# Performance work log

Hardware: AMD Instinct MI355X
Metric: run time of the kernel (lower is better)

The kernel has to match this reference:

```python
import jax, jax.numpy as jnp
import numpy as np

D_MODEL = 1024
NUM_HEADS = 16
HEAD_DIM = D_MODEL // NUM_HEADS  # 64
N = 1024
B = 8


def setup_inputs() -> dict:
    key = jax.random.key(0)
    ks = jax.random.split(key, 11)
    s = 0.02
    inp = {
        'query': jax.random.normal(ks[0], (B, D_MODEL, N), jnp.float32),
        'key':   jax.random.normal(ks[1], (B, D_MODEL, N), jnp.float32),
        'value': jax.random.normal(ks[2], (B, D_MODEL, N), jnp.float32),
        # 1x1 conv1d == linear over channel dim: weight [out, in], bias [out]
        'Wq': jax.random.normal(ks[3], (D_MODEL, D_MODEL), jnp.float32) * s,
        'bq': jax.random.normal(ks[4], (D_MODEL,), jnp.float32) * s,
        'Wk': jax.random.normal(ks[5], (D_MODEL, D_MODEL), jnp.float32) * s,
        'bk': jax.random.normal(ks[6], (D_MODEL,), jnp.float32) * s,
        'Wv': jax.random.normal(ks[7], (D_MODEL, D_MODEL), jnp.float32) * s,
        'bv': jax.random.normal(ks[8], (D_MODEL,), jnp.float32) * s,
        'Wm': jax.random.normal(ks[9], (D_MODEL, D_MODEL), jnp.float32) * s,
        'bm': jax.random.normal(ks[10], (D_MODEL,), jnp.float32) * s,
    }
    return inp


def _proj(W, b, x):
    # nn.Conv1d(kernel_size=1): out[b,o,n] = sum_i W[o,i] x[b,i,n] + b[o]
    return jnp.einsum('oi,bin->bon', W, x) + b[None, :, None]


def reference(query, key, value, Wq, bq, Wk, bk, Wv, bv, Wm, bm):
    Bd = query.shape[0]
    # view(B, dim, heads, N): channel axis split as (head_dim, num_heads)
    q = _proj(Wq, bq, query).reshape(Bd, HEAD_DIM, NUM_HEADS, -1)
    k = _proj(Wk, bk, key).reshape(Bd, HEAD_DIM, NUM_HEADS, -1)
    v = _proj(Wv, bv, value).reshape(Bd, HEAD_DIM, NUM_HEADS, -1)
    scale = 1.0 / (HEAD_DIM ** 0.5)
    scores = jnp.einsum('bdhn,bdhm->bhnm', q, k) * scale  # [B,H,N,N]
    prob = jax.nn.softmax(scores, axis=-1)
    x = jnp.einsum('bhnm,bdhm->bdhn', prob, v)  # [B,D,H,N]
    out = _proj(Wm, bm, x.reshape(Bd, HEAD_DIM * NUM_HEADS, -1))
    return out
```

## Files before the change

kernel.cpp:

```cpp
#include <hip/hip_runtime.h>

typedef __bf16 bf16x8 __attribute__((ext_vector_type(8)));
typedef __bf16 bf16x4 __attribute__((ext_vector_type(4)));
typedef float f32x4 __attribute__((ext_vector_type(4)));
typedef unsigned short u16;
typedef unsigned int u32;

typedef union { bf16x8 v8; bf16x4 v4[2]; } bfu;

__device__ __forceinline__ u16 f2bf(float f) {
  u32 u = __builtin_bit_cast(u32, f);
  u = (u + 0x7FFFu + ((u >> 16) & 1u)) >> 16;
  return (u16)u;
}

__device__ __forceinline__ void gload_lds16(const void* g, void* l) {
  __builtin_amdgcn_global_load_lds((const __attribute__((address_space(1))) void*)g,
                                   (__attribute__((address_space(3))) void*)l, 16, 0, 0);
}

__global__ __launch_bounds__(256) void transpose_cast3(const float* __restrict__ q,
                                                       const float* __restrict__ k,
                                                       const float* __restrict__ v,
                                                       u16* __restrict__ X3) {
  __shared__ float T[64][68];
  int tid = threadIdx.x;
  int n0 = blockIdx.x * 64, i0 = blockIdx.y * 64;
  int z = blockIdx.z;
  int which = z >> 3, b = z & 7;
  const float* src = (which == 0) ? q : (which == 1) ? k : v;
  size_t boff = (size_t)b << 20;
  const float* s = src + boff;
  u16* d = X3 + ((size_t)which << 23) + boff;
  int ir = tid >> 4, n4 = (tid & 15) * 4;
#pragma unroll
  for (int r = 0; r < 4; ++r) {
    int i_loc = ir + r * 16;
    float4 vv = *(const float4*)(s + (size_t)(i0 + i_loc) * 1024 + n0 + n4);
    *(float4*)&T[i_loc][n4] = vv;
  }
  __syncthreads();
  int nr = tid >> 3, i8 = (tid & 7) * 8;
#pragma unroll
  for (int r = 0; r < 2; ++r) {
    int n_loc = nr + r * 32;
    u32 pk[4];
#pragma unroll
    for (int j = 0; j < 4; ++j) {
      float f0 = T[i8 + 2 * j][n_loc];
      float f1 = T[i8 + 2 * j + 1][n_loc];
      pk[j] = (u32)f2bf(f0) | ((u32)f2bf(f1) << 16);
    }
    *(uint4*)(d + (size_t)(n0 + n_loc) * 1024 + i0 + i8) = make_uint4(pk[0], pk[1], pk[2], pk[3]);
  }
}

__global__ __launch_bounds__(256) void transpose_cast(const float* __restrict__ src,
                                                      u16* __restrict__ dst) {
  __shared__ float T[64][68];
  int tid = threadIdx.x;
  int n0 = blockIdx.x * 64, i0 = blockIdx.y * 64;
  size_t boff = (size_t)blockIdx.z << 20;
  const float* s = src + boff;
  u16* d = dst + boff;
  int ir = tid >> 4, n4 = (tid & 15) * 4;
#pragma unroll
  for (int r = 0; r < 4; ++r) {
    int i_loc = ir + r * 16;
    float4 v = *(const float4*)(s + (size_t)(i0 + i_loc) * 1024 + n0 + n4);
    *(float4*)&T[i_loc][n4] = v;
  }
  __syncthreads();
  int nr = tid >> 3, i8 = (tid & 7) * 8;
#pragma unroll
  for (int r = 0; r < 2; ++r) {
    int n_loc = nr + r * 32;
    u32 pk[4];
#pragma unroll
    for (int j = 0; j < 4; ++j) {
      float f0 = T[i8 + 2 * j][n_loc];
      float f1 = T[i8 + 2 * j + 1][n_loc];
      pk[j] = (u32)f2bf(f0) | ((u32)f2bf(f1) << 16);
    }
    *(uint4*)(d + (size_t)(n0 + n_loc) * 1024 + i0 + i8) = make_uint4(pk[0], pk[1], pk[2], pk[3]);
  }
}

__global__ __launch_bounds__(256) void cast_weights(const float* __restrict__ Wq,
                                                    const float* __restrict__ Wk,
                                                    const float* __restrict__ Wv,
                                                    const float* __restrict__ Wm,
                                                    u16* __restrict__ out) {
  int w = blockIdx.y;
  const float* src = (w == 0) ? Wq : (w == 1) ? Wk : (w == 2) ? Wv : Wm;
  u16* dst = out + ((size_t)w << 20);
  int o = blockIdx.x;
  int c4 = threadIdx.x * 4;
  float f[4];
  if (w < 3) {
    float4 v = *(const float4*)(src + (size_t)o * 1024 + c4);
    f[0] = v.x; f[1] = v.y; f[2] = v.z; f[3] = v.w;
  } else {
#pragma unroll
    for (int j = 0; j < 4; ++j) {
      int cp = c4 + j;
      f[j] = src[(size_t)o * 1024 + (cp & 63) * 16 + (cp >> 6)];
    }
  }
  u32 p0 = (u32)f2bf(f[0]) | ((u32)f2bf(f[1]) << 16);
  u32 p1 = (u32)f2bf(f[2]) | ((u32)f2bf(f[3]) << 16);
  *(uint2*)(dst + (size_t)o * 1024 + c4) = make_uint2(p0, p1);
}

__device__ __forceinline__ void gemm_body(const u16* __restrict__ A,
                                          const u16* __restrict__ B,
                                          const float* __restrict__ bias,
                                          void* __restrict__ Out, float escale,
                                          int epi, u16* LD) {
  int tid = threadIdx.x;
  int wave = tid >> 6, l = tid & 63, ln = l & 15, g = l >> 4;
  int wm = wave >> 2, wn = wave & 3;
  int bid = blockIdx.x;
  int mt = (bid >> 3) & 7;
  int nt = ((bid & 7) << 2) | (bid >> 6);
  int c0 = mt * 128, n0 = nt * 256;

  int R = tid >> 3, sl = tid & 7;
  int v = sl ^ (R & 7);
  int sa = v >> 2, sg = v & 3;
  const u16* aSrc = A + (size_t)(c0 + 2 * R + sa) * 1024 + sg * 8;
  const u16* bSrc0 = B + (size_t)(n0 + 2 * R + sa) * 1024 + sg * 8;
  const u16* bSrc1 = B + (size_t)(n0 + 128 + 2 * R + sa) * 1024 + sg * 8;

  int slr = ((((ln & 1) << 2) | g) ^ ((ln >> 1) & 7)) * 8;
  int laneA = (wm * 32 + (ln >> 1)) * 64 + slr;
  int laneB = (wn * 32 + (ln >> 1)) * 64 + slr;

  f32x4 acc[4][4] = {};

#define STAGE(buf, kt)                                                   \
  do {                                                                   \
    gload_lds16(aSrc + (kt) * 32, &LD[(buf) * 4096 + tid * 8]);          \
    gload_lds16(bSrc0 + (kt) * 32, &LD[16384 + (buf) * 8192 + tid * 8]); \
    gload_lds16(bSrc1 + (kt) * 32,                                       \
                &LD[16384 + (buf) * 8192 + 4096 + tid * 8]);             \
  } while (0)

  STAGE(0, 0);
  STAGE(1, 1);
  STAGE(2, 2);

#pragma unroll
  for (int t = 0; t < 32; ++t) {
    if (t < 30)
      asm volatile("s_waitcnt vmcnt(6)" ::: "memory");
    else if (t == 30)
      asm volatile("s_waitcnt vmcnt(3)" ::: "memory");
    else
      asm volatile("s_waitcnt vmcnt(0)" ::: "memory");
    asm volatile("s_barrier" ::: "memory");
    if (t <= 28) STAGE((t + 3) & 3, t + 3);
    const int ab = (t & 3) * 4096;
    const int bb = 16384 + (t & 3) * 8192;
    bf16x8 af[4], bfr[4];
#pragma unroll
    for (int mm = 0; mm < 4; ++mm) af[mm] = *(const bf16x8*)&LD[ab + laneA + mm * 512];
#pragma unroll
    for (int nn = 0; nn < 4; ++nn) bfr[nn] = *(const bf16x8*)&LD[bb + laneB + nn * 512];
    __builtin_amdgcn_s_setprio(1);
#pragma unroll
    for (int mm = 0; mm < 4; ++mm)
#pragma unroll
      for (int nn = 0; nn < 4; ++nn)
        acc[mm][nn] = __builtin_amdgcn_mfma_f32_16x16x32_bf16(af[mm], bfr[nn], acc[mm][nn], 0, 0, 0);
    __builtin_amdgcn_s_setprio(0);
  }
#undef STAGE

  int D0 = (c0 >> 4) + wm * 4;
#pragma unroll
  for (int nn = 0; nn < 4; ++nn) {
    size_t ng = (size_t)n0 + wn * 64 + nn * 16 + ln;
#pragma unroll
    for (int r = 0; r < 4; ++r) {
      int h = g * 4 + r;
      if (epi == 0) {
        bf16x4 pk;
#pragma unroll
        for (int mm = 0; mm < 4; ++mm) {
          int c = c0 + wm * 64 + mm * 16 + h;
          pk[mm] = (__bf16)((acc[mm][nn][r] + bias[c]) * escale);
        }
        *(bf16x4*)((u16*)Out + ng * 1024 + (size_t)h * 64 + D0) = pk;
      } else {
        size_t b = ng >> 10, n = ng & 1023;
#pragma unroll
        for (int mm = 0; mm < 4; ++mm) {
          int c = c0 + wm * 64 + mm * 16 + h;
          float val = (acc[mm][nn][r] + bias[c]) * escale;
          if (epi == 1) {
            int d = D0 + mm;
            ((u16*)Out)[((b * 16 + h) * 64 + d) * 1024 + n] = f2bf(val);
          } else {
            ((float*)Out)[(b << 20) + (size_t)c * 1024 + n] = val;
          }
        }
      }
    }
  }
}

template <int EPI>
__global__ __launch_bounds__(512, 2) void gemm4b(const u16* __restrict__ A,
                                                 const u16* __restrict__ B,
                                                 const float* __restrict__ bias,
                                                 void* __restrict__ Out, float escale) {
  __shared__ u16 LD[49152];
  gemm_body(A, B, bias, Out, escale, EPI, LD);
}

__global__ __launch_bounds__(512, 2) void gemm_qkv(const u16* __restrict__ Wbf,
                                                   const u16* __restrict__ X3,
                                                   const float* __restrict__ bq,
                                                   const float* __restrict__ bk,
                                                   const float* __restrict__ bv,
                                                   u16* __restrict__ Qh,
                                                   u16* __restrict__ Kh,
                                                   u16* __restrict__ Vt, float qscale) {
  __shared__ u16 LD[49152];
  int z = blockIdx.y;
  const u16* A = Wbf + ((size_t)z << 20);
  const u16* B = X3 + ((size_t)z << 23);
  const float* bias = (z == 0) ? bq : (z == 1) ? bk : bv;
  void* Out = (z == 0) ? (void*)Qh : (z == 1) ? (void*)Kh : (void*)Vt;
  float escale = (z == 0) ? qscale : 1.0f;
  int epi = (z == 2) ? 1 : 0;
  gemm_body(A, B, bias, Out, escale, epi, LD);
}

__global__ __launch_bounds__(256, 4) void attn_kernel(const u16* __restrict__ Qh,
                                                      const u16* __restrict__ Kh,
                                                      const u16* __restrict__ Vt,
                                                      u16* __restrict__ Xh) {
  __shared__ u16 Ks[2][4096];
  __shared__ u16 Vs[2][4096];
  int tid = threadIdx.x;
  int w = tid >> 6, l = tid & 63, ln = l & 15, g = l >> 4;
  int id = blockIdx.x;
  int qp = (id & 63) >> 3;
  int bh = ((id >> 6) << 3) | (id & 7);
  size_t b = bh >> 4;
  int h = bh & 15;
  const u16* Qg = Qh + (b << 20) + (h << 6);
  const u16* Kg = Kh + (b << 20) + (h << 6);
  const u16* Vg = Vt + ((size_t)bh << 16);
  u16* Og = Xh + (b << 20) + (h << 6);

  bf16x8 qf[2][2];
#pragma unroll
  for (int t = 0; t < 2; ++t)
#pragma unroll
    for (int kk = 0; kk < 2; ++kk)
      qf[t][kk] = *(const bf16x8*)(Qg + (size_t)(qp * 128 + t * 64 + w * 16 + ln) * 1024 + kk * 32 + g * 8);

  int lr = l >> 3;
  int sw8 = ((l & 7) ^ lr) << 3;
  int r0 = w * 16 + lr, r1 = r0 + 8;
  const u16* kS0 = Kg + (size_t)r0 * 1024 + sw8;
  const u16* kS1 = Kg + (size_t)r1 * 1024 + sw8;
  const u16* vS0 = Vg + (size_t)r0 * 1024 + sw8;
  const u16* vS1 = Vg + (size_t)r1 * 1024 + sw8;

  f32x4 xacc[2][4] = {};
  float lacc[2] = {0.f, 0.f};

  gload_lds16(kS0, &Ks[0][(w * 2) * 512]);
  gload_lds16(kS1, &Ks[0][(w * 2 + 1) * 512]);
  gload_lds16(vS0, &Vs[0][(w * 2) * 512]);
  gload_lds16(vS1, &Vs[0][(w * 2 + 1) * 512]);
  __syncthreads();

  int sx = ln & 7;
  int cur = 0;
  for (int kt = 0; kt < 16; ++kt) {
    if (kt < 15) {
      int nxt = cur ^ 1;
      gload_lds16(kS0 + (size_t)(kt + 1) * 65536, &Ks[nxt][(w * 2) * 512]);
      gload_lds16(kS1 + (size_t)(kt + 1) * 65536, &Ks[nxt][(w * 2 + 1) * 512]);
      gload_lds16(vS0 + (kt + 1) * 64, &Vs[nxt][(w * 2) * 512]);
      gload_lds16(vS1 + (kt + 1) * 64, &Vs[nxt][(w * 2 + 1) * 512]);
    }
    bf16x8 kf[2][4];
#pragma unroll
    for (int kk = 0; kk < 2; ++kk)
#pragma unroll
      for (int f = 0; f < 4; ++f) {
        int slot = (((kk << 2) + g) ^ sx) << 3;
        kf[kk][f] = *(const bf16x8*)&Ks[cur][(f * 16 + ln) * 64 + slot];
      }
    bf16x8 vf[2][4];
#pragma unroll
    for (int kk = 0; kk < 2; ++kk) {
      int s0 = (kk << 2) + (g >> 1);
      int off = (g & 1) << 2;
#pragma unroll
      for (int fd = 0; fd < 4; ++fd) {
        int rowb = (fd * 16 + ln) * 64;
        bfu uv;
        uv.v4[0] = *(const bf16x4*)&Vs[cur][rowb + ((s0 ^ sx) << 3) + off];
        uv.v4[1] = *(const bf16x4*)&Vs[cur][rowb + (((s0 + 2) ^ sx) << 3) + off];
        vf[kk][fd] = uv.v8;
      }
    }
    f32x4 sacc[2][4] = {};
#pragma unroll
    for (int t = 0; t < 2; ++t)
#pragma unroll
      for (int kk = 0; kk < 2; ++kk)
#pragma unroll
        for (int f = 0; f < 4; ++f)
          sacc[t][f] = __builtin_amdgcn_mfma_f32_16x16x32_bf16(kf[kk][f], qf[t][kk], sacc[t][f], 0, 0, 0);
#pragma unroll
    for (int t = 0; t < 2; ++t) {
      bf16x8 pf[2];
#pragma unroll
      for (int kk = 0; kk < 2; ++kk) {
        bfu up;
#pragma unroll
        for (int e2 = 0; e2 < 2; ++e2) {
          int f = 2 * kk + e2;
          float p0 = __builtin_amdgcn_exp2f(sacc[t][f][0]);
          float p1 = __builtin_amdgcn_exp2f(sacc[t][f][1]);
          float p2 = __builtin_amdgcn_exp2f(sacc[t][f][2]);
          float p3 = __builtin_amdgcn_exp2f(sacc[t][f][3]);
          lacc[t] += (p0 + p1) + (p2 + p3);
          bf16x4 pb;
          pb[0] = (__bf16)p0; pb[1] = (__bf16)p1; pb[2] = (__bf16)p2; pb[3] = (__bf16)p3;
          up.v4[e2] = pb;
        }
        pf[kk] = up.v8;
      }
#pragma unroll
      for (int kk = 0; kk < 2; ++kk)
#pragma unroll
        for (int fd = 0; fd < 4; ++fd)
          xacc[t][fd] = __builtin_amdgcn_mfma_f32_16x16x32_bf16(pf[kk], vf[kk][fd], xacc[t][fd], 0, 0, 0);
    }
    __syncthreads();
    cur ^= 1;
  }

#pragma unroll
  for (int t = 0; t < 2; ++t) {
    float lt = lacc[t];
    lt += __shfl_xor(lt, 16);
    lt += __shfl_xor(lt, 32);
    float il[4];
#pragma unroll
    for (int r = 0; r < 4; ++r) il[r] = 1.0f / __shfl(lt, g * 4 + r);
#pragma unroll
    for (int fd = 0; fd < 4; ++fd)
#pragma unroll
      for (int r = 0; r < 4; ++r) {
        int nq = qp * 128 + t * 64 + w * 16 + g * 4 + r;
        Og[(size_t)nq * 1024 + fd * 16 + ln] = f2bf(xacc[t][fd][r] * il[r]);
      }
  }
}

extern "C" void kernel_launch(void* const* d_in, const int* in_sizes, int n_in,
                              void* d_out, int out_size, void* d_ws, size_t ws_size,
                              hipStream_t stream) {
  const float* q  = (const float*)d_in[0];
  const float* k  = (const float*)d_in[1];
  const float* v  = (const float*)d_in[2];
  const float* Wq = (const float*)d_in[3];
  const float* bq = (const float*)d_in[4];
  const float* Wk = (const float*)d_in[5];
  const float* bk = (const float*)d_in[6];
  const float* Wv = (const float*)d_in[7];
  const float* bv = (const float*)d_in[8];
  const float* Wm = (const float*)d_in[9];
  const float* bm = (const float*)d_in[10];

  char* ws = (char*)d_ws;
  u16* Wbf = (u16*)ws;
  u16* Qh  = (u16*)(ws + (8ull << 20));
  u16* Kh  = (u16*)(ws + (24ull << 20));
  u16* Vt  = (u16*)(ws + (40ull << 20));
  u16* X3  = (u16*)(ws + (56ull << 20));

  cast_weights<<<dim3(1024, 4, 1), 256, 0, stream>>>(Wq, Wk, Wv, Wm, Wbf);

  const float qscale = 0.125f * 1.44269504088896340736f;

  if (ws_size >= (104ull << 20)) {
    transpose_cast3<<<dim3(16, 16, 24), 256, 0, stream>>>(q, k, v, X3);
    gemm_qkv<<<dim3(256, 3), 512, 0, stream>>>(Wbf, X3, bq, bk, bv, Qh, Kh, Vt, qscale);
  } else {
    dim3 tg(16, 16, 8);
    transpose_cast<<<tg, 256, 0, stream>>>(q, X3);
    gemm4b<0><<<256, 512, 0, stream>>>(Wbf, X3, bq, Qh, qscale);
    transpose_cast<<<tg, 256, 0, stream>>>(k, X3);
    gemm4b<0><<<256, 512, 0, stream>>>(Wbf + (1u << 20), X3, bk, Kh, 1.0f);
    transpose_cast<<<tg, 256, 0, stream>>>(v, X3);
    gemm4b<1><<<256, 512, 0, stream>>>(Wbf + (2u << 20), X3, bv, Vt, 1.0f);
  }

  attn_kernel<<<1024, 256, 0, stream>>>(Qh, Kh, Vt, X3);

  gemm4b<2><<<256, 512, 0, stream>>>(Wbf + (3u << 20), X3, bm, d_out, 1.0f);
}
```

Baseline: 180.8 us.

## Enlarge GEMM tiles to 256x256 with new LDS swizzle and halved grid

Switches the projection GEMMs from 128x256 to 256x256 output tiles per block, doubling A-side staging and accumulators per wave (8x4 MFMA tiles) and reworking the LDS swizzle and tile-to-block mapping. The aim is more operand reuse per LDS load and fewer global loads per FLOP. In exchange it halves the number of blocks to 128 per GEMM, raises LDS use to 128KB per block, and increases register pressure. Together these can reduce occupancy and leave many CUs idle.

```diff
diff --git a/kernel.cpp b/kernel.cpp
--- a/kernel.cpp
+++ b/kernel.cpp
@@ -112,72 +112,73 @@
   *(uint2*)(dst + (size_t)o * 1024 + c4) = make_uint2(p0, p1);
 }
 
-__device__ __forceinline__ void gemm_body(const u16* __restrict__ A,
-                                          const u16* __restrict__ B,
-                                          const float* __restrict__ bias,
-                                          void* __restrict__ Out, float escale,
-                                          int epi, u16* LD) {
+__device__ __forceinline__ void gemm256_body(const u16* __restrict__ A,
+                                             const u16* __restrict__ B,
+                                             const float* __restrict__ bias,
+                                             void* __restrict__ Out, float escale,
+                                             int epi, u16* LD) {
   int tid = threadIdx.x;
   int wave = tid >> 6, l = tid & 63, ln = l & 15, g = l >> 4;
   int wm = wave >> 2, wn = wave & 3;
   int bid = blockIdx.x;
-  int mt = (bid >> 3) & 7;
-  int nt = ((bid & 7) << 2) | (bid >> 6);
-  int c0 = mt * 128, n0 = nt * 256;
-
-  int R = tid >> 3, sl = tid & 7;
-  int v = sl ^ (R & 7);
-  int sa = v >> 2, sg = v & 3;
-  const u16* aSrc = A + (size_t)(c0 + 2 * R + sa) * 1024 + sg * 8;
-  const u16* bSrc0 = B + (size_t)(n0 + 2 * R + sa) * 1024 + sg * 8;
-  const u16* bSrc1 = B + (size_t)(n0 + 128 + 2 * R + sa) * 1024 + sg * 8;
-
-  int slr = ((((ln & 1) << 2) | g) ^ ((ln >> 1) & 7)) * 8;
-  int laneA = (wm * 32 + (ln >> 1)) * 64 + slr;
-  int laneB = (wn * 32 + (ln >> 1)) * 64 + slr;
-
-  f32x4 acc[4][4] = {};
-
-#define STAGE(buf, kt)                                                   \
+  int work = (bid & 7) * 16 + (bid >> 3);
+  int mt = work >> 5, nt = work & 31;
+  int c0 = mt * 256, n0 = nt * 256;
+
+  int r0 = tid >> 2, cs = tid & 3;
+  int col0 = (cs ^ ((r0 & 3) ^ ((r0 >> 2) & 3))) * 8;
+  const u16* aS0 = A + (size_t)(c0 + r0) * 1024 + col0;
+  const u16* aS1 = A + (size_t)(c0 + 128 + r0) * 1024 + col0;
+  const u16* bS0 = B + (size_t)(n0 + r0) * 1024 + col0;
+  const u16* bS1 = B + (size_t)(n0 + 128 + r0) * 1024 + col0;
+
+  int sl = (g ^ (ln & 3) ^ ((ln >> 2) & 3)) * 8;
+  int laneA = (wm * 128 + ln) * 32 + sl;
+  int laneB = (wn * 64 + ln) * 32 + sl;
+
+  f32x4 acc[8][4] = {};
+
+#define STG(buf, kt)                                                     \
   do {                                                                   \
-    gload_lds16(aSrc + (kt) * 32, &LD[(buf) * 4096 + tid * 8]);          \
-    gload_lds16(bSrc0 + (kt) * 32, &LD[16384 + (buf) * 8192 + tid * 8]); \
-    gload_lds16(bSrc1 + (kt) * 32,                                       \
-                &LD[16384 + (buf) * 8192 + 4096 + tid * 8]);             \
+    gload_lds16(aS0 + (kt) * 32, &LD[(buf) * 8192 + tid * 8]);           \
+    gload_lds16(aS1 + (kt) * 32, &LD[(buf) * 8192 + 4096 + tid * 8]);    \
+    gload_lds16(bS0 + (kt) * 32, &LD[32768 + (buf) * 8192 + tid * 8]);   \
+    gload_lds16(bS1 + (kt) * 32,                                         \
+                &LD[32768 + (buf) * 8192 + 4096 + tid * 8]);             \
   } while (0)
 
-  STAGE(0, 0);
-  STAGE(1, 1);
-  STAGE(2, 2);
+  STG(0, 0);
+  STG(1, 1);
+  STG(2, 2);
 
 #pragma unroll
   for (int t = 0; t < 32; ++t) {
     if (t < 30)
-      asm volatile("s_waitcnt vmcnt(6)" ::: "memory");
+      asm volatile("s_waitcnt vmcnt(8)" ::: "memory");
     else if (t == 30)
-      asm volatile("s_waitcnt vmcnt(3)" ::: "memory");
+      asm volatile("s_waitcnt vmcnt(4)" ::: "memory");
     else
       asm volatile("s_waitcnt vmcnt(0)" ::: "memory");
     asm volatile("s_barrier" ::: "memory");
-    if (t <= 28) STAGE((t + 3) & 3, t + 3);
-    const int ab = (t & 3) * 4096;
-    const int bb = 16384 + (t & 3) * 8192;
-    bf16x8 af[4], bfr[4];
-#pragma unroll
-    for (int mm = 0; mm < 4; ++mm) af[mm] = *(const bf16x8*)&LD[ab + laneA + mm * 512];
+    if (t <= 28) STG((t + 3) & 3, t + 3);
+    const int ab = (t & 3) * 8192;
+    const int bb = 32768 + (t & 3) * 8192;
+    bf16x8 bfr[4];
 #pragma unroll
     for (int nn = 0; nn < 4; ++nn) bfr[nn] = *(const bf16x8*)&LD[bb + laneB + nn * 512];
     __builtin_amdgcn_s_setprio(1);
 #pragma unroll
-    for (int mm = 0; mm < 4; ++mm)
+    for (int mm = 0; mm < 8; ++mm) {
+      bf16x8 af = *(const bf16x8*)&LD[ab + laneA + mm * 512];
 #pragma unroll
       for (int nn = 0; nn < 4; ++nn)
-        acc[mm][nn] = __builtin_amdgcn_mfma_f32_16x16x32_bf16(af[mm], bfr[nn], acc[mm][nn], 0, 0, 0);
+        acc[mm][nn] = __builtin_amdgcn_mfma_f32_16x16x32_bf16(af, bfr[nn], acc[mm][nn], 0, 0, 0);
+    }
     __builtin_amdgcn_s_setprio(0);
   }
-#undef STAGE
-
-  int D0 = (c0 >> 4) + wm * 4;
+#undef STG
+
+  int D0 = (c0 >> 4) + wm * 8;
 #pragma unroll
   for (int nn = 0; nn < 4; ++nn) {
     size_t ng = (size_t)n0 + wn * 64 + nn * 16 + ln;
@@ -185,18 +186,18 @@
     for (int r = 0; r < 4; ++r) {
       int h = g * 4 + r;
       if (epi == 0) {
-        bf16x4 pk;
-#pragma unroll
-        for (int mm = 0; mm < 4; ++mm) {
-          int c = c0 + wm * 64 + mm * 16 + h;
+        bf16x8 pk;
+#pragma unroll
+        for (int mm = 0; mm < 8; ++mm) {
+          int c = c0 + wm * 128 + mm * 16 + h;
           pk[mm] = (__bf16)((acc[mm][nn][r] + bias[c]) * escale);
         }
-        *(bf16x4*)((u16*)Out + ng * 1024 + (size_t)h * 64 + D0) = pk;
+        *(bf16x8*)((u16*)Out + ng * 1024 + (size_t)h * 64 + D0) = pk;
       } else {
         size_t b = ng >> 10, n = ng & 1023;
 #pragma unroll
-        for (int mm = 0; mm < 4; ++mm) {
-          int c = c0 + wm * 64 + mm * 16 + h;
+        for (int mm = 0; mm < 8; ++mm) {
+          int c = c0 + wm * 128 + mm * 16 + h;
           float val = (acc[mm][nn][r] + bias[c]) * escale;
           if (epi == 1) {
             int d = D0 + mm;
@@ -211,12 +212,12 @@
 }
 
 template <int EPI>
-__global__ __launch_bounds__(512, 2) void gemm4b(const u16* __restrict__ A,
-                                                 const u16* __restrict__ B,
-                                                 const float* __restrict__ bias,
-                                                 void* __restrict__ Out, float escale) {
-  __shared__ u16 LD[49152];
-  gemm_body(A, B, bias, Out, escale, EPI, LD);
+__global__ __launch_bounds__(512, 2) void gemm256(const u16* __restrict__ A,
+                                                  const u16* __restrict__ B,
+                                                  const float* __restrict__ bias,
+                                                  void* __restrict__ Out, float escale) {
+  __shared__ u16 LD[65536];
+  gemm256_body(A, B, bias, Out, escale, EPI, LD);
 }
 
 __global__ __launch_bounds__(512, 2) void gemm_qkv(const u16* __restrict__ Wbf,
@@ -227,7 +228,7 @@
                                                    u16* __restrict__ Qh,
                                                    u16* __restrict__ Kh,
                                                    u16* __restrict__ Vt, float qscale) {
-  __shared__ u16 LD[49152];
+  __shared__ u16 LD[65536];
   int z = blockIdx.y;
   const u16* A = Wbf + ((size_t)z << 20);
   const u16* B = X3 + ((size_t)z << 23);
@@ -235,7 +236,7 @@
   void* Out = (z == 0) ? (void*)Qh : (z == 1) ? (void*)Kh : (void*)Vt;
   float escale = (z == 0) ? qscale : 1.0f;
   int epi = (z == 2) ? 1 : 0;
-  gemm_body(A, B, bias, Out, escale, epi, LD);
+  gemm256_body(A, B, bias, Out, escale, epi, LD);
 }
 
 __global__ __launch_bounds__(256, 4) void attn_kernel(const u16* __restrict__ Qh,
@@ -396,18 +397,18 @@
 
   if (ws_size >= (104ull << 20)) {
     transpose_cast3<<<dim3(16, 16, 24), 256, 0, stream>>>(q, k, v, X3);
-    gemm_qkv<<<dim3(256, 3), 512, 0, stream>>>(Wbf, X3, bq, bk, bv, Qh, Kh, Vt, qscale);
+    gemm_qkv<<<dim3(128, 3), 512, 0, stream>>>(Wbf, X3, bq, bk, bv, Qh, Kh, Vt, qscale);
   } else {
     dim3 tg(16, 16, 8);
     transpose_cast<<<tg, 256, 0, stream>>>(q, X3);
-    gemm4b<0><<<256, 512, 0, stream>>>(Wbf, X3, bq, Qh, qscale);
+    gemm256<0><<<128, 512, 0, stream>>>(Wbf, X3, bq, Qh, qscale);
     transpose_cast<<<tg, 256, 0, stream>>>(k, X3);
-    gemm4b<0><<<256, 512, 0, stream>>>(Wbf + (1u << 20), X3, bk, Kh, 1.0f);
+    gemm256<0><<<128, 512, 0, stream>>>(Wbf + (1u << 20), X3, bk, Kh, 1.0f);
     transpose_cast<<<tg, 256, 0, stream>>>(v, X3);
-    gemm4b<1><<<256, 512, 0, stream>>>(Wbf + (2u << 20), X3, bv, Vt, 1.0f);
+    gemm256<1><<<128, 512, 0, stream>>>(Wbf + (2u << 20), X3, bv, Vt, 1.0f);
   }
 
   attn_kernel<<<1024, 256, 0, stream>>>(Qh, Kh, Vt, X3);
 
-  gemm4b<2><<<256, 512, 0, stream>>>(Wbf + (3u << 20), X3, bm, d_out, 1.0f);
-}
+  gemm256<2><<<128, 512, 0, stream>>>(Wbf + (3u << 20), X3, bm, d_out, 1.0f);
+}
```

Result: slower. 203.2 us (+12.4%).
